# Kernel tuning notes

Measured on AMD Instinct MI355X. Metric: run time of the kernel, lower is better.

## Reference

```python
import jax, jax.numpy as jnp
import numpy as np

N_NODES = 100000
N_EDGES = 1600000
NUM_GRAPHS = 256


def _gcn_conv(x, src, dst, deg_isqrt, deg_inv, W, b):
    # GCNConv with self-loops and symmetric normalization (PyG semantics):
    # out_i = sum_{j->i} d_j^-1/2 d_i^-1/2 (x_j W) + d_i^-1 (x_i W) + b
    xl = x @ W  # [N, out]
    norm = deg_isqrt[src] * deg_isqrt[dst]  # [E]
    msgs = norm[:, None] * xl[src]  # [E, out] -- dominant memory traffic
    agg = jax.ops.segment_sum(msgs, dst, num_segments=N_NODES)
    return agg + deg_inv[:, None] * xl + b


def setup_inputs() -> dict:
    key = jax.random.key(0)
    ks = jax.random.split(key, 8)
    F_in, H, T = 128, 128, 64
    x = jax.random.normal(ks[0], (N_NODES, F_in), dtype=jnp.float32)
    edge_index = jax.random.randint(ks[1], (2, N_EDGES), 0, N_NODES, dtype=jnp.int64)
    batch = jnp.sort(jax.random.randint(ks[2], (N_NODES,), 0, NUM_GRAPHS, dtype=jnp.int64))
    s0 = 1.0 / np.sqrt(F_in)
    s1 = 1.0 / np.sqrt(H)
    return {
        "x": x,
        "edge_index": edge_index,
        "batch": batch,
        "W0": jax.random.normal(ks[3], (F_in, H), dtype=jnp.float32) * s0,
        "b0": jnp.zeros((H,), dtype=jnp.float32),
        "W1": jax.random.normal(ks[4], (H, H), dtype=jnp.float32) * s1,
        "b1": jnp.zeros((H,), dtype=jnp.float32),
        "W2": jax.random.normal(ks[5], (H, T), dtype=jnp.float32) * s1,
        "b2": jnp.zeros((T,), dtype=jnp.float32),
    }


def reference(x, edge_index, batch, W0, b0, W1, b1, W2, b2):
    src, dst = edge_index[0], edge_index[1]
    # degree including self-loop
    deg = jax.ops.segment_sum(jnp.ones((N_EDGES,), x.dtype), dst, num_segments=N_NODES) + 1.0
    deg_isqrt = jax.lax.rsqrt(deg)
    deg_inv = 1.0 / deg

    h = jax.nn.gelu(_gcn_conv(x, src, dst, deg_isqrt, deg_inv, W0, b0))
    h = jax.nn.gelu(_gcn_conv(h, src, dst, deg_isqrt, deg_inv, W1, b1))
    h = jax.nn.gelu(_gcn_conv(h, src, dst, deg_isqrt, deg_inv, W2, b2))

    # global_mean_pool over graphs
    sums = jax.ops.segment_sum(h, batch, num_segments=NUM_GRAPHS)
    counts = jax.ops.segment_sum(jnp.ones((N_NODES,), h.dtype), batch, num_segments=NUM_GRAPHS)
    return sums / jnp.maximum(counts, 1.0)[:, None]
```

## Files before the change

### kernel.cpp

```cpp
#include <hip/hip_runtime.h>
#include <math.h>

#define F_IN 128
#define TDIM 64
#define NGRAPH 256

typedef __attribute__((ext_vector_type(8))) short short8;
typedef __attribute__((ext_vector_type(4))) float f32x4;
typedef __attribute__((ext_vector_type(2))) __fp16 fp16x2;

__device__ __forceinline__ float gelu_f(float x) {
    float x3 = x * x * x;
    return 0.5f * x * (1.0f + tanhf(0.7978845608028654f * (x + 0.044715f * x3)));
}

__device__ __forceinline__ unsigned short bf16_of(float x) {
    unsigned u = __float_as_uint(x);
    return (unsigned short)((u + 0x7fffu + ((u >> 16) & 1u)) >> 16);
}
__device__ __forceinline__ float f_of(unsigned short h) {
    return __uint_as_float(((unsigned)h) << 16);
}
__device__ __forceinline__ unsigned bf16pair(float a, float b) {
    return (unsigned)bf16_of(a) | ((unsigned)bf16_of(b) << 16);
}
__device__ __forceinline__ float2 bf16unpack(unsigned u) {
    float2 r;
    r.x = __uint_as_float(u << 16);
    r.y = __uint_as_float(u & 0xffff0000u);
    return r;
}

__device__ __forceinline__ unsigned pkf16(float a, float b) {
    fp16x2 h = __builtin_amdgcn_cvt_pkrtz(a, b);
    return __builtin_bit_cast(unsigned, h);
}
__device__ __forceinline__ float2 f16unpack(unsigned u) {
    fp16x2 h = __builtin_bit_cast(fp16x2, u);
    float2 r;
    r.x = (float)h[0];
    r.y = (float)h[1];
    return r;
}

__device__ __forceinline__ void fmix2(float& ax, float& ay, unsigned pk, float nw) {
    asm("v_fma_mix_f32 %0, %1, %2, %0 op_sel:[0,0,0] op_sel_hi:[1,0,0]"
        : "+v"(ax)
        : "v"(pk), "v"(nw));
    asm("v_fma_mix_f32 %0, %1, %2, %0 op_sel:[1,0,0] op_sel_hi:[1,0,0]"
        : "+v"(ay)
        : "v"(pk), "v"(nw));
}


#define BIN_CH 4096
#define MAXNB 512
#define CAP 6144

__global__ __launch_bounds__(256) void zero_kernel(float* __restrict__ psum,
                                                   float* __restrict__ pcnt,
                                                   int* __restrict__ bucket_cnt) {
    int i = blockIdx.x * 256 + threadIdx.x;
    if (i < NGRAPH * TDIM) psum[i] = 0.f;
    if (i < NGRAPH) pcnt[i] = 0.f;
    if (i < MAXNB) bucket_cnt[i] = 0;
}

__global__ __launch_bounds__(256) void binC_kernel(const int* __restrict__ src,
                                                   const int* __restrict__ dst,
                                                   int* __restrict__ bucket_cnt,
                                                   unsigned* __restrict__ tmp, int E, int NB) {
    __shared__ int hist[MAXNB];
    __shared__ int hbase[MAXNB];
    __shared__ int hcur[MAXNB];
    int tid = threadIdx.x;
    int base = blockIdx.x * BIN_CH;
    int end = base + BIN_CH;
    if (end > E) end = E;
    for (int i = tid; i < NB; i += 256) hist[i] = 0;
    __syncthreads();
    for (int e = base + tid; e < end; e += 256) atomicAdd(&hist[dst[e] >> 8], 1);
    __syncthreads();
    for (int i = tid; i < NB; i += 256) {
        int c = hist[i];
        hbase[i] = (c > 0) ? atomicAdd(&bucket_cnt[i], c) : 0;
        hcur[i] = 0;
    }
    __syncthreads();
    for (int e = base + tid; e < end; e += 256) {
        int d = dst[e];
        int b = d >> 8;
        int p = atomicAdd(&hcur[b], 1);
        int slot = hbase[b] + p;
        if (slot < CAP)
            tmp[(size_t)b * CAP + slot] = (unsigned)src[e] | ((unsigned)(d & 255) << 24);
    }
}

__global__ __launch_bounds__(256) void scan_wconv_kernel(const int* __restrict__ bucket_cnt,
                                                         int* __restrict__ bbase,
                                                         int* __restrict__ row_off, int NB,
                                                         int N, const float* __restrict__ W0,
                                                         const float* __restrict__ W1,
                                                         const float* __restrict__ W2,
                                                         unsigned short* __restrict__ hi0,
                                                         unsigned short* __restrict__ lo0,
                                                         unsigned short* __restrict__ hi1,
                                                         unsigned short* __restrict__ lo1,
                                                         unsigned short* __restrict__ hi2,
                                                         unsigned short* __restrict__ lo2) {
    if (blockIdx.x == 0) {
        __shared__ int sh[256];
        int tid = threadIdx.x;
        int i0 = tid * 2;
        int v0 = 0, v1 = 0;
        if (i0 < NB) {
            v0 = bucket_cnt[i0];
            v0 = v0 < CAP ? v0 : CAP;
        }
        if (i0 + 1 < NB) {
            v1 = bucket_cnt[i0 + 1];
            v1 = v1 < CAP ? v1 : CAP;
        }
        int s = v0 + v1;
        sh[tid] = s;
        __syncthreads();
        for (int off = 1; off < 256; off <<= 1) {
            int x = (tid >= off) ? sh[tid - off] : 0;
            __syncthreads();
            sh[tid] += x;
            __syncthreads();
        }
        int excl = sh[tid] - s;
        if (i0 < NB) bbase[i0] = excl;
        if (i0 + 1 < NB) bbase[i0 + 1] = excl + v0;
        if (tid == 255) row_off[N] = sh[255];
        return;
    }
    int idx = (blockIdx.x - 1) * 256 + threadIdx.x;
    const float* W;
    unsigned short *whi, *wlo;
    int local, FOUT;
    if (idx < 16384) {
        W = W0; whi = hi0; wlo = lo0; local = idx; FOUT = 128;
    } else if (idx < 32768) {
        W = W1; whi = hi1; wlo = lo1; local = idx - 16384; FOUT = 128;
    } else if (idx < 40960) {
        W = W2; whi = hi2; wlo = lo2; local = idx - 32768; FOUT = 64;
    } else {
        return;
    }
    int k = local / FOUT;
    int n = local % FOUT;
    float w = W[local];
    unsigned short h = bf16_of(w);
    whi[(size_t)n * 128 + k] = h;
    wlo[(size_t)n * 128 + k] = bf16_of(w - f_of(h));
}

__global__ __launch_bounds__(256) void binDcount_kernel(const unsigned* __restrict__ tmp,
                                                        const int* __restrict__ bucket_cnt,
                                                        const int* __restrict__ bbase,
                                                        int* __restrict__ row_off,
                                                        float* __restrict__ isq,
                                                        float* __restrict__ dinv, int N) {
    __shared__ int lcnt[256];
    __shared__ int sh[256];
    int b = blockIdx.x;
    int tid = threadIdx.x;
    int cntb = bucket_cnt[b];
    if (cntb > CAP) cntb = CAP;
    lcnt[tid] = 0;
    __syncthreads();
    const unsigned* tb = tmp + (size_t)b * CAP;
    for (int e = tid; e < cntb; e += 256) atomicAdd(&lcnt[tb[e] >> 24], 1);
    __syncthreads();
    int own = lcnt[tid];
    sh[tid] = own;
    __syncthreads();
    for (int off = 1; off < 256; off <<= 1) {
        int x = (tid >= off) ? sh[tid - off] : 0;
        __syncthreads();
        sh[tid] += x;
        __syncthreads();
    }
    int excl = sh[tid] - own;
    int node = (b << 8) + tid;
    if (node < N) {
        row_off[node] = bbase[b] + excl;
        float d = (float)own + 1.0f;
        isq[node] = rsqrtf(d);
        dinv[node] = 1.0f / d;
    }
}

__global__ __launch_bounds__(256) void binDscatter_kernel(const unsigned* __restrict__ tmp,
                                                          const int* __restrict__ bucket_cnt,
                                                          const int* __restrict__ row_off,
                                                          const float* __restrict__ isq,
                                                          uint2* __restrict__ edges, int N) {
    __shared__ int lcur[256];
    __shared__ float lisq[256];
    int b = blockIdx.x;
    int node0 = b << 8;
    int tid = threadIdx.x;
    lcur[tid] = 0;
    int nd = node0 + tid;
    lisq[tid] = (nd < N) ? isq[nd] : 0.f;
    __syncthreads();
    int cntb = bucket_cnt[b];
    if (cntb > CAP) cntb = CAP;
    const unsigned* tb = tmp + (size_t)b * CAP;
    for (int e = tid; e < cntb; e += 256) {
        unsigned rec = tb[e];
        int dl = (int)(rec >> 24);
        unsigned s = rec & 0xFFFFFFu;
        int p = atomicAdd(&lcur[dl], 1);
        float nrm = isq[s] * lisq[dl];
        edges[(size_t)row_off[node0 + dl] + p] = make_uint2(s, __float_as_uint(nrm));
    }
}


#define LROW 136

__global__ __launch_bounds__(256) void gemm_f32_kernel(const float* __restrict__ X,
                                                       const unsigned short* __restrict__ whiT,
                                                       const unsigned short* __restrict__ wloT,
                                                       unsigned* __restrict__ Yb, int nrows) {
    constexpr int FOUT = 128;
    constexpr int NT = FOUT / 16;
    __shared__ short lds[2 * FOUT * LROW];
    short* shi = lds;
    short* slo = lds + FOUT * LROW;

    for (int c = threadIdx.x; c < FOUT * 16; c += 256) {
        int n = c >> 4, r = c & 15;
        *(short8*)(shi + n * LROW + r * 8) = *(const short8*)(whiT + (size_t)n * 128 + r * 8);
        *(short8*)(slo + n * LROW + r * 8) = *(const short8*)(wloT + (size_t)n * 128 + r * 8);
    }
    __syncthreads();

    int lane = threadIdx.x & 63;
    int wave = threadIdx.x >> 6;
    int quad = lane >> 4;
    int l16 = lane & 15;
    int rowBase = blockIdx.x * 256 + wave * 64;

    f32x4 acc[4][NT];
#pragma unroll
    for (int m = 0; m < 4; ++m)
#pragma unroll
        for (int t = 0; t < NT; ++t) acc[m][t] = (f32x4){0.f, 0.f, 0.f, 0.f};

    const float* xr[4];
    bool ok[4];
#pragma unroll
    for (int m = 0; m < 4; ++m) {
        int arow = rowBase + m * 16 + l16;
        ok[m] = arow < nrows;
        xr[m] = X + (size_t)arow * 128;
    }

#pragma unroll
    for (int k0 = 0; k0 < 128; k0 += 32) {
        short8 ahi[4], alo[4];
#pragma unroll
        for (int m = 0; m < 4; ++m) {
            float xv[8];
            if (ok[m]) {
                float4 v0 = *(const float4*)(xr[m] + k0 + quad * 8);
                float4 v1 = *(const float4*)(xr[m] + k0 + quad * 8 + 4);
                xv[0] = v0.x; xv[1] = v0.y; xv[2] = v0.z; xv[3] = v0.w;
                xv[4] = v1.x; xv[5] = v1.y; xv[6] = v1.z; xv[7] = v1.w;
            } else {
#pragma unroll
                for (int j = 0; j < 8; ++j) xv[j] = 0.f;
            }
#pragma unroll
            for (int j = 0; j < 8; ++j) {
                unsigned short h = bf16_of(xv[j]);
                ahi[m][j] = (short)h;
                alo[m][j] = (short)bf16_of(xv[j] - f_of(h));
            }
        }
#pragma unroll
        for (int t = 0; t < NT; ++t) {
            int off = (t * 16 + l16) * LROW + k0 + quad * 8;
            short8 bhi = *(const short8*)(shi + off);
            short8 blo = *(const short8*)(slo + off);
#pragma unroll
            for (int m = 0; m < 4; ++m) {
                acc[m][t] = __builtin_amdgcn_mfma_f32_16x16x32_bf16(ahi[m], bhi, acc[m][t], 0, 0, 0);
                acc[m][t] = __builtin_amdgcn_mfma_f32_16x16x32_bf16(alo[m], bhi, acc[m][t], 0, 0, 0);
                acc[m][t] = __builtin_amdgcn_mfma_f32_16x16x32_bf16(ahi[m], blo, acc[m][t], 0, 0, 0);
            }
        }
    }

#pragma unroll
    for (int m = 0; m < 4; ++m) {
#pragma unroll
        for (int t = 0; t < NT; ++t) {
            int col = t * 16 + l16;
#pragma unroll
            for (int i = 0; i < 4; ++i) {
                int r = rowBase + m * 16 + quad * 4 + i;
                float v = acc[m][t][i];
                float nb = __shfl_xor(v, 1, 64);
                if (((lane & 1) == 0) && r < nrows)
                    Yb[(size_t)r * (FOUT / 2) + (col >> 1)] = pkf16(v, nb);
            }
        }
    }
}


template <int FOUT>
__global__ __launch_bounds__(256) void gemm_bf16_kernel(const unsigned* __restrict__ Xb,
                                                        const unsigned short* __restrict__ whiT,
                                                        unsigned* __restrict__ Yb, int nrows) {
    constexpr int NT = FOUT / 16;
    __shared__ short shi[FOUT * LROW];

    for (int c = threadIdx.x; c < FOUT * 16; c += 256) {
        int n = c >> 4, r = c & 15;
        *(short8*)(shi + n * LROW + r * 8) = *(const short8*)(whiT + (size_t)n * 128 + r * 8);
    }
    __syncthreads();

    int lane = threadIdx.x & 63;
    int wave = threadIdx.x >> 6;
    int quad = lane >> 4;
    int l16 = lane & 15;
    int rowBase = blockIdx.x * 256 + wave * 64;

    f32x4 acc[4][NT];
#pragma unroll
    for (int m = 0; m < 4; ++m)
#pragma unroll
        for (int t = 0; t < NT; ++t) acc[m][t] = (f32x4){0.f, 0.f, 0.f, 0.f};

    const short* xs[4];
    bool ok[4];
#pragma unroll
    for (int m = 0; m < 4; ++m) {
        int arow = rowBase + m * 16 + l16;
        ok[m] = arow < nrows;
        xs[m] = (const short*)Xb + (size_t)arow * 128;
    }

#pragma unroll
    for (int k0 = 0; k0 < 128; k0 += 32) {
        short8 a[4];
#pragma unroll
        for (int m = 0; m < 4; ++m) {
            if (ok[m])
                a[m] = *(const short8*)(xs[m] + k0 + quad * 8);
            else
                a[m] = (short8){0, 0, 0, 0, 0, 0, 0, 0};
        }
#pragma unroll
        for (int t = 0; t < NT; ++t) {
            short8 b = *(const short8*)(shi + (t * 16 + l16) * LROW + k0 + quad * 8);
#pragma unroll
            for (int m = 0; m < 4; ++m)
                acc[m][t] = __builtin_amdgcn_mfma_f32_16x16x32_bf16(a[m], b, acc[m][t], 0, 0, 0);
        }
    }

#pragma unroll
    for (int m = 0; m < 4; ++m) {
#pragma unroll
        for (int t = 0; t < NT; ++t) {
            int col = t * 16 + l16;
#pragma unroll
            for (int i = 0; i < 4; ++i) {
                int r = rowBase + m * 16 + quad * 4 + i;
                float v = acc[m][t][i];
                float nb = __shfl_xor(v, 1, 64);
                if (((lane & 1) == 0) && r < nrows)
                    Yb[(size_t)r * (FOUT / 2) + (col >> 1)] = pkf16(v, nb);
            }
        }
    }
}


__global__ __launch_bounds__(256) void agg128_kernel(const unsigned* __restrict__ xlb,
                                                     const int* __restrict__ row_off,
                                                     const uint2* __restrict__ edges,
                                                     const float* __restrict__ dinv,
                                                     const float* __restrict__ bias,
                                                     unsigned* __restrict__ outb, int nnodes) {
    int wave = (blockIdx.x * blockDim.x + threadIdx.x) >> 6;
    int lane = threadIdx.x & 63;
    if (wave >= nnodes) return;
    int e0 = __builtin_amdgcn_readfirstlane(row_off[wave]);
    int e1 = __builtin_amdgcn_readfirstlane(row_off[wave + 1]);
    float ax = 0.f, ay = 0.f;
    int e = e0;
    int l16 = lane & 15;
    int nfull = (e1 - e0) >> 4;
    for (int r = 0; r < nfull; ++r, e += 16) {
        uint2 edv = edges[e + l16];
        unsigned pk[16];
        float nw[16];
#pragma unroll
        for (int j = 0; j < 16; ++j) {
            int sx = __builtin_amdgcn_readlane((int)edv.x, j);
            nw[j] = __uint_as_float((unsigned)__builtin_amdgcn_ds_bpermute(j * 4, (int)edv.y));
            pk[j] = xlb[(size_t)(unsigned)sx * 64 + lane];
        }
#pragma unroll
        for (int j = 0; j < 16; ++j) fmix2(ax, ay, pk[j], nw[j]);
    }
    if (e < e1) {
        int idx = e + l16;
        uint2 edv = edges[idx < e1 ? idx : e1 - 1];
        if (idx >= e1) edv.y = 0u;
        unsigned pk[16];
        float nw[16];
#pragma unroll
        for (int j = 0; j < 16; ++j) {
            int sx = __builtin_amdgcn_readlane((int)edv.x, j);
            nw[j] = __uint_as_float((unsigned)__builtin_amdgcn_ds_bpermute(j * 4, (int)edv.y));
            pk[j] = xlb[(size_t)(unsigned)sx * 64 + lane];
        }
#pragma unroll
        for (int j = 0; j < 16; ++j) fmix2(ax, ay, pk[j], nw[j]);
    }
    float di = dinv[wave];
    float2 pi = f16unpack(xlb[(size_t)wave * 64 + lane]);
    float2 bb = *(const float2*)(bias + lane * 2);
    outb[(size_t)wave * 64 + lane] =
        bf16pair(gelu_f(ax + di * pi.x + bb.x), gelu_f(ay + di * pi.y + bb.y));
}


__global__ __launch_bounds__(256) void agg64_kernel(const unsigned* __restrict__ xlb,
                                                    const int* __restrict__ row_off,
                                                    const uint2* __restrict__ edges,
                                                    const float* __restrict__ dinv,
                                                    const float* __restrict__ bias,
                                                    unsigned* __restrict__ outb, int nnodes) {
    int wave = (blockIdx.x * blockDim.x + threadIdx.x) >> 6;
    int lane = threadIdx.x & 63;
    int sub = lane >> 5;
    int sl = lane & 31;
    int node = wave * 2 + sub;
    bool nv = node < nnodes;
    int e0 = nv ? row_off[node] : 0;
    int e1 = nv ? row_off[node + 1] : 0;
    int rounds = (e1 - e0 + 15) >> 4;
    int ro = __shfl_xor(rounds, 32, 64);
    int maxr = rounds > ro ? rounds : ro;
    float ax = 0.f, ay = 0.f;
    int bidx = (lane & 32) << 2;
    for (int r = 0; r < maxr; ++r) {
        int idx = e0 + (r << 4) + (lane & 15);
        int cl = idx < e1 ? idx : (e1 > e0 ? e1 - 1 : 0);
        uint2 edv = edges[cl];
        if (idx >= e1) edv.y = 0u;
        int sv[16];
        float nw[16];
#pragma unroll
        for (int j = 0; j < 16; ++j) {
            int bj = bidx + j * 4;
            sv[j] = __builtin_amdgcn_ds_bpermute(bj, (int)edv.x);
            nw[j] = __uint_as_float((unsigned)__builtin_amdgcn_ds_bpermute(bj, (int)edv.y));
        }
        unsigned pk[16];
#pragma unroll
        for (int j = 0; j < 16; ++j) pk[j] = xlb[(((unsigned)sv[j]) << 5) + (unsigned)sl];
#pragma unroll
        for (int j = 0; j < 16; ++j) fmix2(ax, ay, pk[j], nw[j]);
    }
    if (nv) {
        float di = dinv[node];
        float2 pi = f16unpack(xlb[(size_t)node * 32 + sl]);
        float2 bb = *(const float2*)(bias + sl * 2);
        outb[(size_t)node * 32 + sl] =
            bf16pair(gelu_f(ax + di * pi.x + bb.x), gelu_f(ay + di * pi.y + bb.y));
    }
}


#define POOL_CHUNK 64

__global__ __launch_bounds__(256) void pool_kernel(const unsigned* __restrict__ hb,
                                                   const int* __restrict__ batch,
                                                   float* __restrict__ psum,
                                                   float* __restrict__ pcnt, int nnodes) {
    int wave = (blockIdx.x * blockDim.x + threadIdx.x) >> 6;
    int lane = threadIdx.x & 63;
    int half = lane >> 5;
    int p = lane & 31;
    int n0 = wave * POOL_CHUNK + half * 32;
    if (n0 >= nnodes) return;
    int n1 = n0 + 32;
    if (n1 > nnodes) n1 = nnodes;

    int g_cur = batch[n0];
    float accx = 0.f, accy = 0.f;
    int cnt = 0;
    for (int node = n0; node < n1; ++node) {
        int g = batch[node];
        if (g != g_cur) {
            atomicAdd(&psum[g_cur * TDIM + 2 * p], accx);
            atomicAdd(&psum[g_cur * TDIM + 2 * p + 1], accy);
            if (p == 0) atomicAdd(&pcnt[g_cur], (float)cnt);
            accx = 0.f;
            accy = 0.f;
            cnt = 0;
            g_cur = g;
        }
        float2 f = bf16unpack(hb[(size_t)node * 32 + p]);
        accx += f.x;
        accy += f.y;
        ++cnt;
    }
    atomicAdd(&psum[g_cur * TDIM + 2 * p], accx);
    atomicAdd(&psum[g_cur * TDIM + 2 * p + 1], accy);
    if (p == 0) atomicAdd(&pcnt[g_cur], (float)cnt);
}

__global__ __launch_bounds__(256) void fin_kernel(const float* __restrict__ psum,
                                                  const float* __restrict__ pcnt,
                                                  float* __restrict__ out) {
    int i = blockIdx.x * blockDim.x + threadIdx.x;
    if (i < NGRAPH * TDIM) {
        float c = pcnt[i >> 6];
        out[i] = psum[i] / fmaxf(c, 1.0f);
    }
}


extern "C" void kernel_launch(void* const* d_in, const int* in_sizes, int n_in,
                              void* d_out, int out_size, void* d_ws, size_t ws_size,
                              hipStream_t stream) {
    const float* x = (const float*)d_in[0];
    const int* ei = (const int*)d_in[1];
    const int* batch = (const int*)d_in[2];
    const float* W0 = (const float*)d_in[3];
    const float* b0 = (const float*)d_in[4];
    const float* W1 = (const float*)d_in[5];
    const float* b1 = (const float*)d_in[6];
    const float* W2 = (const float*)d_in[7];
    const float* b2 = (const float*)d_in[8];

    const int N = in_sizes[0] / F_IN;
    const int E = in_sizes[1] / 2;
    const int* src = ei;
    const int* dst = ei + E;
    const int NB = (N + 255) >> 8;

    char* w = (char*)d_ws;
    auto alloc = [&](size_t bytes) -> void* {
        void* p = (void*)w;
        w += (bytes + 255) & ~(size_t)255;
        return p;
    };
    float* isq = (float*)alloc((size_t)N * 4);
    float* dinv = (float*)alloc((size_t)N * 4);
    int* bucket_cnt = (int*)alloc((size_t)MAXNB * 4);
    int* bbase = (int*)alloc((size_t)MAXNB * 4);
    int* row_off = (int*)alloc((size_t)(N + 1) * 4);
    uint2* edges = (uint2*)alloc((size_t)E * 8);
    unsigned* tmp = (unsigned*)alloc((size_t)NB * CAP * 4);
    float* psum = (float*)alloc((size_t)NGRAPH * TDIM * 4);
    float* pcnt = (float*)alloc((size_t)NGRAPH * 4);
    unsigned* bufXb = (unsigned*)alloc((size_t)N * 64 * 4);
    unsigned* bufHb = (unsigned*)alloc((size_t)N * 64 * 4);
    unsigned short* whiT0 = (unsigned short*)alloc(128 * 128 * 2);
    unsigned short* wloT0 = (unsigned short*)alloc(128 * 128 * 2);
    unsigned short* whiT1 = (unsigned short*)alloc(128 * 128 * 2);
    unsigned short* wloT1 = (unsigned short*)alloc(128 * 128 * 2);
    unsigned short* whiT2 = (unsigned short*)alloc(64 * 128 * 2);
    unsigned short* wloT2 = (unsigned short*)alloc(64 * 128 * 2);

    zero_kernel<<<(NGRAPH * TDIM + 255) / 256, 256, 0, stream>>>(psum, pcnt, bucket_cnt);

    int cblocks = (E + BIN_CH - 1) / BIN_CH;
    binC_kernel<<<cblocks, 256, 0, stream>>>(src, dst, bucket_cnt, tmp, E, NB);
    scan_wconv_kernel<<<1 + (40960 + 255) / 256, 256, 0, stream>>>(
        bucket_cnt, bbase, row_off, NB, N, W0, W1, W2, whiT0, wloT0, whiT1, wloT1, whiT2,
        wloT2);
    binDcount_kernel<<<NB, 256, 0, stream>>>(tmp, bucket_cnt, bbase, row_off, isq, dinv, N);
    binDscatter_kernel<<<NB, 256, 0, stream>>>(tmp, bucket_cnt, row_off, isq, edges, N);

    int gblocks = (N + 255) / 256;
    int ablocks = (N * 64 + 255) / 256;
    int a64blocks = (((N + 1) / 2) * 64 + 255) / 256;

    gemm_f32_kernel<<<gblocks, 256, 0, stream>>>(x, whiT0, wloT0, bufXb, N);
    agg128_kernel<<<ablocks, 256, 0, stream>>>(bufXb, row_off, edges, dinv, b0, bufHb, N);
    gemm_bf16_kernel<128><<<gblocks, 256, 0, stream>>>(bufHb, whiT1, bufXb, N);
    agg128_kernel<<<ablocks, 256, 0, stream>>>(bufXb, row_off, edges, dinv, b1, bufHb, N);
    gemm_bf16_kernel<64><<<gblocks, 256, 0, stream>>>(bufHb, whiT2, bufXb, N);
    agg64_kernel<<<a64blocks, 256, 0, stream>>>(bufXb, row_off, edges, dinv, b2, bufHb, N);

    int pwaves = (N + POOL_CHUNK - 1) / POOL_CHUNK;
    int pblocks = (pwaves * 64 + 255) / 256;
    pool_kernel<<<pblocks, 256, 0, stream>>>(bufHb, batch, psum, pcnt, N);
    fin_kernel<<<(NGRAPH * TDIM + 255) / 256, 256, 0, stream>>>(psum, pcnt, (float*)d_out);
}
```

Before: 386.8 us.

## Slice-major feature layout, packed fp16 edge records, and bias+GELU fused into GEMM

Measured after the change: 831.5 us. 115% more time.

```diff
diff --git a/kernel.cpp b/kernel.cpp
--- a/kernel.cpp
+++ b/kernel.cpp
@@ -51,6 +51,16 @@
         : "+v"(ay)
         : "v"(pk), "v"(nw));
 }
+__device__ __forceinline__ void fmix2h(float& ax, float& ay, unsigned pk, unsigned nw) {
+    asm("v_fma_mix_f32 %0, %1, %2, %0 op_sel:[0,0,0] op_sel_hi:[1,1,0]"
+        : "+v"(ax)
+        : "v"(pk), "v"(nw));
+    asm("v_fma_mix_f32 %0, %1, %2, %0 op_sel:[1,0,0] op_sel_hi:[1,1,0]"
+        : "+v"(ay)
+        : "v"(pk), "v"(nw));
+}
+
+#define REP16(M) M(0) M(1) M(2) M(3) M(4) M(5) M(6) M(7) M(8) M(9) M(10) M(11) M(12) M(13) M(14) M(15)
 
 
 #define BIN_CH 4096
@@ -198,7 +208,7 @@
                                                           const int* __restrict__ bucket_cnt,
                                                           const int* __restrict__ row_off,
                                                           const float* __restrict__ isq,
-                                                          uint2* __restrict__ edges, int N) {
+                                                          unsigned* __restrict__ edgesP, int N) {
     __shared__ int lcur[256];
     __shared__ float lisq[256];
     int b = blockIdx.x;
@@ -217,7 +227,9 @@
         unsigned s = rec & 0xFFFFFFu;
         int p = atomicAdd(&lcur[dl], 1);
         float nrm = isq[s] * lisq[dl];
-        edges[(size_t)row_off[node0 + dl] + p] = make_uint2(s, __float_as_uint(nrm));
+        __fp16 hn = (__fp16)nrm;
+        unsigned hb = (unsigned)__builtin_bit_cast(unsigned short, hn);
+        edgesP[(size_t)row_off[node0 + dl] + p] = s | (hb << 17);
     }
 }
 
@@ -227,7 +239,7 @@
 __global__ __launch_bounds__(256) void gemm_f32_kernel(const float* __restrict__ X,
                                                        const unsigned short* __restrict__ whiT,
                                                        const unsigned short* __restrict__ wloT,
-                                                       unsigned* __restrict__ Yb, int nrows) {
+                                                       unsigned* __restrict__ YbS, int nrows) {
     constexpr int FOUT = 128;
     constexpr int NT = FOUT / 16;
     __shared__ short lds[2 * FOUT * LROW];
@@ -246,6 +258,7 @@
     int quad = lane >> 4;
     int l16 = lane & 15;
     int rowBase = blockIdx.x * 256 + wave * 64;
+    size_t sstride = (size_t)nrows * 8;
 
     f32x4 acc[4][NT];
 #pragma unroll
@@ -302,14 +315,13 @@
     for (int m = 0; m < 4; ++m) {
 #pragma unroll
         for (int t = 0; t < NT; ++t) {
-            int col = t * 16 + l16;
 #pragma unroll
             for (int i = 0; i < 4; ++i) {
                 int r = rowBase + m * 16 + quad * 4 + i;
                 float v = acc[m][t][i];
                 float nb = __shfl_xor(v, 1, 64);
                 if (((lane & 1) == 0) && r < nrows)
-                    Yb[(size_t)r * (FOUT / 2) + (col >> 1)] = pkf16(v, nb);
+                    YbS[(size_t)t * sstride + (size_t)r * 8 + (l16 >> 1)] = pkf16(v, nb);
             }
         }
     }
@@ -317,8 +329,9 @@
 
 
 template <int FOUT>
-__global__ __launch_bounds__(256) void gemm_bf16_kernel(const unsigned* __restrict__ Xb,
+__global__ __launch_bounds__(256) void gemm_bf16_kernel(const unsigned* __restrict__ XbS,
                                                         const unsigned short* __restrict__ whiT,
+                                                        const float* __restrict__ bias_prev,
                                                         unsigned* __restrict__ Yb, int nrows) {
     constexpr int NT = FOUT / 16;
     __shared__ short shi[FOUT * LROW];
@@ -334,6 +347,7 @@
     int quad = lane >> 4;
     int l16 = lane & 15;
     int rowBase = blockIdx.x * 256 + wave * 64;
+    size_t sstride = (size_t)nrows * 8;
 
     f32x4 acc[4][NT];
 #pragma unroll
@@ -341,24 +355,40 @@
 #pragma unroll
         for (int t = 0; t < NT; ++t) acc[m][t] = (f32x4){0.f, 0.f, 0.f, 0.f};
 
-    const short* xs[4];
+    int arow[4];
     bool ok[4];
 #pragma unroll
     for (int m = 0; m < 4; ++m) {
-        int arow = rowBase + m * 16 + l16;
-        ok[m] = arow < nrows;
-        xs[m] = (const short*)Xb + (size_t)arow * 128;
+        arow[m] = rowBase + m * 16 + l16;
+        ok[m] = arow[m] < nrows;
     }
 
 #pragma unroll
     for (int k0 = 0; k0 < 128; k0 += 32) {
+        int c = (k0 >> 3) + quad;
+        const float4* bp = (const float4*)(bias_prev + c * 8);
+        float4 bv0 = bp[0], bv1 = bp[1];
+        float bb[8] = {bv0.x, bv0.y, bv0.z, bv0.w, bv1.x, bv1.y, bv1.z, bv1.w};
         short8 a[4];
 #pragma unroll
         for (int m = 0; m < 4; ++m) {
-            if (ok[m])
-                a[m] = *(const short8*)(xs[m] + k0 + quad * 8);
-            else
+            if (ok[m]) {
+                const uint4 v = *(const uint4*)(XbS + (size_t)(c >> 1) * sstride +
+                                                (size_t)arow[m] * 8 + (c & 1) * 4);
+                unsigned vw[4] = {v.x, v.y, v.z, v.w};
+                unsigned* ap = (unsigned*)&a[m];
+#pragma unroll
+                for (int jw = 0; jw < 4; ++jw) {
+                    float2 f = f16unpack(vw[jw]);
+                    float g0 = gelu_f(f.x + bb[jw * 2]);
+                    float g1 = gelu_f(f.y + bb[jw * 2 + 1]);
+                    unsigned aw;
+                    asm("v_cvt_pk_bf16_f32 %0, %1, %2" : "=v"(aw) : "v"(g0), "v"(g1));
+                    ap[jw] = aw;
+                }
+            } else {
                 a[m] = (short8){0, 0, 0, 0, 0, 0, 0, 0};
+            }
         }
 #pragma unroll
         for (int t = 0; t < NT; ++t) {
@@ -373,74 +403,73 @@
     for (int m = 0; m < 4; ++m) {
 #pragma unroll
         for (int t = 0; t < NT; ++t) {
-            int col = t * 16 + l16;
 #pragma unroll
             for (int i = 0; i < 4; ++i) {
                 int r = rowBase + m * 16 + quad * 4 + i;
                 float v = acc[m][t][i];
                 float nb = __shfl_xor(v, 1, 64);
-                if (((lane & 1) == 0) && r < nrows)
-                    Yb[(size_t)r * (FOUT / 2) + (col >> 1)] = pkf16(v, nb);
+                if (((lane & 1) == 0) && r < nrows) {
+                    if (FOUT == 128) {
+                        Yb[(size_t)t * sstride + (size_t)r * 8 + (l16 >> 1)] = pkf16(v, nb);
+                    } else {
+                        int col = t * 16 + l16;
+                        Yb[(size_t)r * (FOUT / 2) + (col >> 1)] = pkf16(v, nb);
+                    }
+                }
             }
         }
     }
 }
 
 
-__global__ __launch_bounds__(256) void agg128_kernel(const unsigned* __restrict__ xlb,
-                                                     const int* __restrict__ row_off,
-                                                     const uint2* __restrict__ edges,
-                                                     const float* __restrict__ dinv,
-                                                     const float* __restrict__ bias,
-                                                     unsigned* __restrict__ outb, int nnodes) {
-    int wave = (blockIdx.x * blockDim.x + threadIdx.x) >> 6;
+__global__ __launch_bounds__(256) void agg128s_kernel(const unsigned* __restrict__ xlbS,
+                                                      const int* __restrict__ row_off,
+                                                      const unsigned* __restrict__ edgesP,
+                                                      const float* __restrict__ dinv,
+                                                      unsigned* __restrict__ outS, int nnodes) {
+    int s = blockIdx.x & 7;
+    int node = (blockIdx.x >> 3) * 4 + (threadIdx.x >> 6);
+    if (node >= nnodes) return;
     int lane = threadIdx.x & 63;
-    if (wave >= nnodes) return;
-    int e0 = __builtin_amdgcn_readfirstlane(row_off[wave]);
-    int e1 = __builtin_amdgcn_readfirstlane(row_off[wave + 1]);
+    int g = lane >> 3;
+    int w = lane & 7;
+    size_t sbase = (size_t)s * ((size_t)nnodes * 8);
+    const unsigned* arena = xlbS + sbase;
+    int e0 = __builtin_amdgcn_readfirstlane(row_off[node]);
+    int e1 = __builtin_amdgcn_readfirstlane(row_off[node + 1]);
     float ax = 0.f, ay = 0.f;
-    int e = e0;
-    int l16 = lane & 15;
-    int nfull = (e1 - e0) >> 4;
-    for (int r = 0; r < nfull; ++r, e += 16) {
-        uint2 edv = edges[e + l16];
-        unsigned pk[16];
-        float nw[16];
-#pragma unroll
-        for (int j = 0; j < 16; ++j) {
-            int sx = __builtin_amdgcn_readlane((int)edv.x, j);
-            nw[j] = __uint_as_float((unsigned)__builtin_amdgcn_ds_bpermute(j * 4, (int)edv.y));
-            pk[j] = xlb[(size_t)(unsigned)sx * 64 + lane];
-        }
-#pragma unroll
-        for (int j = 0; j < 16; ++j) fmix2(ax, ay, pk[j], nw[j]);
-    }
-    if (e < e1) {
-        int idx = e + l16;
-        uint2 edv = edges[idx < e1 ? idx : e1 - 1];
-        if (idx >= e1) edv.y = 0u;
-        unsigned pk[16];
-        float nw[16];
-#pragma unroll
-        for (int j = 0; j < 16; ++j) {
-            int sx = __builtin_amdgcn_readlane((int)edv.x, j);
-            nw[j] = __uint_as_float((unsigned)__builtin_amdgcn_ds_bpermute(j * 4, (int)edv.y));
-            pk[j] = xlb[(size_t)(unsigned)sx * 64 + lane];
-        }
-#pragma unroll
-        for (int j = 0; j < 16; ++j) fmix2(ax, ay, pk[j], nw[j]);
-    }
-    float di = dinv[wave];
-    float2 pi = f16unpack(xlb[(size_t)wave * 64 + lane]);
-    float2 bb = *(const float2*)(bias + lane * 2);
-    outb[(size_t)wave * 64 + lane] =
-        bf16pair(gelu_f(ax + di * pi.x + bb.x), gelu_f(ay + di * pi.y + bb.y));
-}
-
+    for (int base = e0; base < e1; base += 8) {
+        int idx = base + g;
+        int cl = idx < e1 ? idx : e1 - 1;
+        unsigned rec = __builtin_nontemporal_load(edgesP + cl);
+        if (idx >= e1) rec = 0u;
+        unsigned nw = rec >> 17;
+        unsigned src = rec & 0x1FFFFu;
+        unsigned pk = arena[src * 8 + (unsigned)w];
+        fmix2h(ax, ay, pk, nw);
+    }
+    ax += __shfl_xor(ax, 8, 64);
+    ay += __shfl_xor(ay, 8, 64);
+    ax += __shfl_xor(ax, 16, 64);
+    ay += __shfl_xor(ay, 16, 64);
+    ax += __shfl_xor(ax, 32, 64);
+    ay += __shfl_xor(ay, 32, 64);
+    if (g == 0) {
+        float di = dinv[node];
+        unsigned pkSelf = arena[(size_t)node * 8 + w];
+        fmix2(ax, ay, pkSelf, di);
+        __builtin_nontemporal_store(pkf16(ax, ay), outS + sbase + (size_t)node * 8 + w);
+    }
+}
+
+
+#define A64_BP(j) unsigned rv##j = (unsigned)__builtin_amdgcn_ds_bpermute(bidx + 4 * j, (int)rec);
+#define A64_GL(j) unsigned pk##j = xlb[((rv##j & 0x1FFFFu) << 5) + (unsigned)sl];
+#define A64_FM(j) fmix2h(ax, ay, pk##j, rv##j >> 17);
 
 __global__ __launch_bounds__(256) void agg64_kernel(const unsigned* __restrict__ xlb,
                                                     const int* __restrict__ row_off,
-                                                    const uint2* __restrict__ edges,
+                                                    const unsigned* __restrict__ edgesP,
                                                     const float* __restrict__ dinv,
                                                     const float* __restrict__ bias,
                                                     unsigned* __restrict__ outb, int nnodes) {
@@ -460,21 +489,11 @@
     for (int r = 0; r < maxr; ++r) {
         int idx = e0 + (r << 4) + (lane & 15);
         int cl = idx < e1 ? idx : (e1 > e0 ? e1 - 1 : 0);
-        uint2 edv = edges[cl];
-        if (idx >= e1) edv.y = 0u;
-        int sv[16];
-        float nw[16];
-#pragma unroll
-        for (int j = 0; j < 16; ++j) {
-            int bj = bidx + j * 4;
-            sv[j] = __builtin_amdgcn_ds_bpermute(bj, (int)edv.x);
-            nw[j] = __uint_as_float((unsigned)__builtin_amdgcn_ds_bpermute(bj, (int)edv.y));
-        }
-        unsigned pk[16];
-#pragma unroll
-        for (int j = 0; j < 16; ++j) pk[j] = xlb[(((unsigned)sv[j]) << 5) + (unsigned)sl];
-#pragma unroll
-        for (int j = 0; j < 16; ++j) fmix2(ax, ay, pk[j], nw[j]);
+        unsigned rec = edgesP[cl];
+        if (idx >= e1) rec = 0u;
+        REP16(A64_BP)
+        REP16(A64_GL)
+        REP16(A64_FM)
     }
     if (nv) {
         float di = dinv[node];
@@ -566,7 +585,7 @@
     int* bucket_cnt = (int*)alloc((size_t)MAXNB * 4);
     int* bbase = (int*)alloc((size_t)MAXNB * 4);
     int* row_off = (int*)alloc((size_t)(N + 1) * 4);
-    uint2* edges = (uint2*)alloc((size_t)E * 8);
+    unsigned* edgesP = (unsigned*)alloc((size_t)E * 4);
     unsigned* tmp = (unsigned*)alloc((size_t)NB * CAP * 4);
     float* psum = (float*)alloc((size_t)NGRAPH * TDIM * 4);
     float* pcnt = (float*)alloc((size_t)NGRAPH * 4);
@@ -587,18 +606,18 @@
         bucket_cnt, bbase, row_off, NB, N, W0, W1, W2, whiT0, wloT0, whiT1, wloT1, whiT2,
         wloT2);
     binDcount_kernel<<<NB, 256, 0, stream>>>(tmp, bucket_cnt, bbase, row_off, isq, dinv, N);
-    binDscatter_kernel<<<NB, 256, 0, stream>>>(tmp, bucket_cnt, row_off, isq, edges, N);
+    binDscatter_kernel<<<NB, 256, 0, stream>>>(tmp, bucket_cnt, row_off, isq, edgesP, N);
 
     int gblocks = (N + 255) / 256;
-    int ablocks = (N * 64 + 255) / 256;
+    int asblocks = 8 * ((N + 3) / 4);
     int a64blocks = (((N + 1) / 2) * 64 + 255) / 256;
 
     gemm_f32_kernel<<<gblocks, 256, 0, stream>>>(x, whiT0, wloT0, bufXb, N);
-    agg128_kernel<<<ablocks, 256, 0, stream>>>(bufXb, row_off, edges, dinv, b0, bufHb, N);
-    gemm_bf16_kernel<128><<<gblocks, 256, 0, stream>>>(bufHb, whiT1, bufXb, N);
-    agg128_kernel<<<ablocks, 256, 0, stream>>>(bufXb, row_off, edges, dinv, b1, bufHb, N);
-    gemm_bf16_kernel<64><<<gblocks, 256, 0, stream>>>(bufHb, whiT2, bufXb, N);
-    agg64_kernel<<<a64blocks, 256, 0, stream>>>(bufXb, row_off, edges, dinv, b2, bufHb, N);
+    agg128s_kernel<<<asblocks, 256, 0, stream>>>(bufXb, row_off, edgesP, dinv, bufHb, N);
+    gemm_bf16_kernel<128><<<gblocks, 256, 0, stream>>>(bufHb, whiT1, b0, bufXb, N);
+    agg128s_kernel<<<asblocks, 256, 0, stream>>>(bufXb, row_off, edgesP, dinv, bufHb, N);
+    gemm_bf16_kernel<64><<<gblocks, 256, 0, stream>>>(bufHb, whiT2, b1, bufXb, N);
+    agg64_kernel<<<a64blocks, 256, 0, stream>>>(bufXb, row_off, edgesP, dinv, b2, bufHb, N);
 
     int pwaves = (N + POOL_CHUNK - 1) / POOL_CHUNK;
     int pblocks = (pwaves * 64 + 255) / 256;
```
